# Kernel optimization log

Measured on AMD Instinct MI355X. Metric: run time of the kernel, lower is better.

Reference implementation:

```python
import jax, jax.numpy as jnp
import numpy as np

# dims: N batch, C in-channels, T frames, V joints, H heads, HD per-head dim, O out-channels
N, C, T, V = 32, 64, 256, 25
H, HD, O = 8, 8, 64  # HD = max(C//8, 8)
SCALE = HD ** -0.5
EPS = 1e-5


def setup_inputs() -> dict:
    key = jax.random.key(0)
    ks = jax.random.split(key, 10)
    return {
        "x": jax.random.normal(ks[0], (N, C, T, V), jnp.float32),
        "ln_gamma": jnp.ones((C,), jnp.float32),
        "ln_beta": jnp.zeros((C,), jnp.float32),
        "w_qk": jax.random.normal(ks[1], (C, 2 * H * HD), jnp.float32),  # to_qk init N(0,1)
        "b_qk": jax.random.normal(ks[2], (2 * H * HD,), jnp.float32) * 0.02,
        "shared_topology": jax.random.uniform(ks[3], (H, V, V), jnp.float32),
        "conv_w": jax.random.normal(ks[4], (H, O, C), jnp.float32) * np.sqrt(2.0 / (O * H)),
        "conv_b": jnp.zeros((H, O), jnp.float32),
        "bn_gamma": jnp.full((O,), 1e-6, jnp.float32),
        "bn_beta": jnp.zeros((O,), jnp.float32),
        "bn_mean": jnp.zeros((O,), jnp.float32),
        "bn_var": jnp.ones((O,), jnp.float32),
    }


def reference(x, ln_gamma, ln_beta, w_qk, b_qk, shared_topology,
              conv_w, conv_b, bn_gamma, bn_beta, bn_mean, bn_var):
    # ---- SelfAttention over joints ----
    y = jnp.transpose(x, (0, 2, 3, 1))                 # [N,T,V,C]
    mu = jnp.mean(y, axis=-1, keepdims=True)
    var = jnp.var(y, axis=-1, keepdims=True)
    yn = (y - mu) * jax.lax.rsqrt(var + EPS) * ln_gamma + ln_beta
    qk = yn @ w_qk + b_qk                              # [N,T,V,2*H*HD]
    B = N * T
    q, k = jnp.split(qk.reshape(B, V, 2 * H * HD), 2, axis=-1)
    q = q.reshape(B, V, H, HD).transpose(0, 2, 1, 3)   # [B,H,V,HD]
    k = k.reshape(B, V, H, HD).transpose(0, 2, 1, 3)
    dots = jnp.einsum("bhid,bhjd->bhij", q, k) * SCALE
    attn = jax.nn.softmax(dots, axis=-1).astype(jnp.float32)  # [B,H,V,V]

    # ---- attention-gated graph conv ----
    A = attn * shared_topology[None]                   # [B,H,V,V]
    feat = jnp.transpose(x, (0, 2, 3, 1)).reshape(B, V, C)  # [B,V,C]
    z = jnp.einsum("bhuv,bvc->bhuc", A, feat)          # per-head aggregate [B,H,V,C]
    # fused per-head 1x1 convs + sum over heads
    out = jnp.einsum("bhuc,hoc->buo", z, conv_w) + conv_b.sum(0)  # [B,V,O]
    out = out.reshape(N, T, V, O).transpose(0, 3, 1, 2)           # [N,O,T,V]

    # ---- BatchNorm (inference-mode) + residual + ReLU ----
    g = (bn_gamma * jax.lax.rsqrt(bn_var + EPS))[None, :, None, None]
    b = (bn_beta - bn_mean * bn_gamma * jax.lax.rsqrt(bn_var + EPS))[None, :, None, None]
    out = out * g + b
    out = jax.nn.relu(out + x)  # down is identity (in_c == out_c)
    return out
```

## Files before the change

### kernel.cpp

```cpp
#include <hip/hip_runtime.h>
#include <math.h>

#define SCALE 0.35355339059327373f
#define EPSV 1e-5f

typedef __attribute__((ext_vector_type(8))) short bf16x8;
typedef __attribute__((ext_vector_type(4))) float f32x4;
typedef __attribute__((ext_vector_type(16))) float f32x16;
typedef __attribute__((ext_vector_type(4))) int i32x4;
typedef __attribute__((ext_vector_type(2))) int i32x2;

static __device__ __forceinline__ unsigned short bfh(float f) {
    return (unsigned short)(__builtin_bit_cast(unsigned int, f) >> 16);
}
static __device__ __forceinline__ float bf2f(unsigned short s) {
    return __builtin_bit_cast(float, (unsigned int)s << 16);
}
static __device__ __forceinline__ int pack2(float lo, float hi) {
    return __builtin_amdgcn_perm(__builtin_bit_cast(unsigned int, hi),
                                 __builtin_bit_cast(unsigned int, lo), 0x07060302u);
}
#define LGKM0() __asm__ __volatile__("s_waitcnt lgkmcnt(0)" ::: "memory")

__global__ void prep_kernel(const float* __restrict__ w_qk,
                            const float* __restrict__ conv_w,
                            const float* __restrict__ conv_b,
                            const float* __restrict__ bn_g, const float* __restrict__ bn_b,
                            const float* __restrict__ bn_m, const float* __restrict__ bn_v,
                            unsigned short* __restrict__ ws) {
    int i = blockIdx.x * 256 + threadIdx.x;
    if (i < 8192) {
        int f = i >> 9, rem = i & 511, l = rem >> 3, j = rem & 7;
        int nt = f >> 1, ks = f & 1;
        int k = ks * 32 + (l >> 4) * 8 + j;
        int nn = nt * 16 + (l & 15);
        ws[i] = bfh(w_qk[k * 128 + nn]);
    } else if (i < 40960) {
        int i2 = i - 8192;
        int g = i2 >> 9, rem = i2 & 511, l = rem >> 3, j = rem & 7;
        int h = g >> 3, nt = (g >> 1) & 3, ks = g & 1;
        int c = ks * 32 + (l >> 4) * 8 + j;
        int o = nt * 16 + (l & 15);
        ws[i] = bfh(conv_w[h * 4096 + o * 64 + c]);
    } else if (i < 41024) {
        int o = i - 40960;
        float gv = bn_g[o] * rsqrtf(bn_v[o] + EPSV);
        float bb = bn_b[o] - bn_m[o] * gv;
        float cb = 0.f;
        for (int h = 0; h < 8; h++) cb += conv_b[h * 64 + o];
        float* wsf = (float*)(ws + 40960);
        wsf[o] = gv;
        wsf[64 + o] = bb + cb * gv;
    }
}

__global__ __launch_bounds__(256, 3)
void sagc_kernel(const float* __restrict__ x,
                 const float* __restrict__ ln_g, const float* __restrict__ ln_b,
                 const float* __restrict__ b_qk,
                 const float* __restrict__ topo,
                 const unsigned short* __restrict__ ws,
                 float* __restrict__ out)
{
    __shared__ __align__(16) unsigned char smem[53248];
    const int tid = threadIdx.x;
    const int lane = tid & 63, wv = tid >> 6;
    const int l15 = lane & 15, quad = lane >> 4;
    const int r32 = lane & 31, hi = lane >> 5;

    unsigned char* my = smem + wv * 13312;
    unsigned short* xb16 = (unsigned short*)my;
    unsigned short* FWT  = (unsigned short*)my;
    float*          mus  = (float*)(my + 5120);
    float*          rss  = mus + 32;
    unsigned short* qbuf = (unsigned short*)(my + 5120);
    unsigned short* kbuf = (unsigned short*)(my + 6656);
    unsigned short* Gh   = (unsigned short*)(my + 8192);

    const unsigned short* wqk = ws;
    const unsigned short* w2f = ws + 8192;
    const float* bnA = (const float*)(ws + 40960);
    const float* bnB = bnA + 64;

    const int tile = blockIdx.x * 4 + wv;
    const int n = tile >> 8, t = tile & 255;
    const float* xg = x + (size_t)n * 409600 + (size_t)t * 25;
    float* og = out + (size_t)n * 409600 + (size_t)t * 25;

    #pragma unroll
    for (int it = 0; it < 25; it++) {
        int i = it * 64 + lane;
        int c = i / 25, v = i - c * 25;
        xb16[v * 72 + c] = bfh(xg[c * 6400 + v]);
    }
    #pragma unroll
    for (int k = 0; k < 8; k++) {
        int idx = k * 64 + lane;
        if (idx < 504) {
            int rr = idx / 72, cc = idx - rr * 72;
            xb16[(25 + rr) * 72 + cc] = 0;
        }
    }
    LGKM0();

    bf16x8 xa[2][2];
    #pragma unroll
    for (int mt = 0; mt < 2; mt++)
        #pragma unroll
        for (int ks = 0; ks < 2; ks++)
            xa[mt][ks] = *(const bf16x8*)&xb16[(mt * 16 + l15) * 72 + ks * 32 + quad * 8];

    float xf[2][2][8];
    bf16x8 sqf[2][2];
    #pragma unroll
    for (int mt = 0; mt < 2; mt++)
        #pragma unroll
        for (int ks = 0; ks < 2; ks++) {
            float s[8];
            #pragma unroll
            for (int j = 0; j < 8; j++) {
                xf[mt][ks][j] = bf2f((unsigned short)xa[mt][ks][j]);
                s[j] = xf[mt][ks][j] * xf[mt][ks][j];
            }
            i32x4 p;
            #pragma unroll
            for (int q = 0; q < 4; q++) p[q] = pack2(s[2 * q], s[2 * q + 1]);
            sqf[mt][ks] = __builtin_bit_cast(bf16x8, p);
        }

    {
        i32x4 ones_i = {0x3C803C80, 0x3C803C80, 0x3C803C80, 0x3C803C80};
        bf16x8 onesf = __builtin_bit_cast(bf16x8, ones_i);
        f32x4 z4 = {0.f, 0.f, 0.f, 0.f};
        f32x4 dmu[2], ds2[2];
        #pragma unroll
        for (int mt = 0; mt < 2; mt++) {
            dmu[mt] = __builtin_amdgcn_mfma_f32_16x16x32_bf16(xa[mt][0], onesf, z4, 0, 0, 0);
            dmu[mt] = __builtin_amdgcn_mfma_f32_16x16x32_bf16(xa[mt][1], onesf, dmu[mt], 0, 0, 0);
            ds2[mt] = __builtin_amdgcn_mfma_f32_16x16x32_bf16(sqf[mt][0], onesf, z4, 0, 0, 0);
            ds2[mt] = __builtin_amdgcn_mfma_f32_16x16x32_bf16(sqf[mt][1], onesf, ds2[mt], 0, 0, 0);
        }
        if (l15 == 0) {
            #pragma unroll
            for (int mt = 0; mt < 2; mt++)
                #pragma unroll
                for (int r = 0; r < 4; r++) {
                    int v = mt * 16 + quad * 4 + r;
                    float mu = dmu[mt][r];
                    float var = ds2[mt][r] - mu * mu;
                    mus[v] = mu;
                    rss[v] = rsqrtf(var + EPSV);
                }
        }
    }
    LGKM0();

    bf16x8 yna[2][2];
    {
        float muv[2] = {mus[l15], mus[16 + l15]};
        float rsv[2] = {rss[l15], rss[16 + l15]};
        #pragma unroll
        for (int ks = 0; ks < 2; ks++) {
            f32x4 ga = *(const f32x4*)&ln_g[ks * 32 + quad * 8];
            f32x4 gb = *(const f32x4*)&ln_g[ks * 32 + quad * 8 + 4];
            f32x4 ba = *(const f32x4*)&ln_b[ks * 32 + quad * 8];
            f32x4 bb = *(const f32x4*)&ln_b[ks * 32 + quad * 8 + 4];
            #pragma unroll
            for (int mt = 0; mt < 2; mt++) {
                float yv[8];
                #pragma unroll
                for (int j = 0; j < 8; j++) {
                    float g = (j < 4) ? ga[j] : gb[j - 4];
                    float bt = (j < 4) ? ba[j] : bb[j - 4];
                    yv[j] = (xf[mt][ks][j] - muv[mt]) * rsv[mt] * g + bt;
                }
                i32x4 p;
                #pragma unroll
                for (int q = 0; q < 4; q++) p[q] = pack2(yv[2 * q], yv[2 * q + 1]);
                yna[mt][ks] = __builtin_bit_cast(bf16x8, p);
            }
        }
    }

    f32x4 acc[2][4];
    #pragma unroll
    for (int mt = 0; mt < 2; mt++)
        #pragma unroll
        for (int nt = 0; nt < 4; nt++)
            acc[mt][nt] = (f32x4){0.f, 0.f, 0.f, 0.f};

    const f32x4 z4 = {0.f, 0.f, 0.f, 0.f};
    const bf16x8 z8 = {0, 0, 0, 0, 0, 0, 0, 0};

    for (int hp = 0; hp < 4; hp++) {
        #pragma unroll
        for (int tsel = 0; tsel < 2; tsel++) {
            int nt = tsel ? (4 + hp) : hp;
            bf16x8 b0 = *(const bf16x8*)&wqk[(nt * 2 + 0) * 512 + lane * 8];
            bf16x8 b1 = *(const bf16x8*)&wqk[(nt * 2 + 1) * 512 + lane * 8];
            float bias = b_qk[(tsel ? 64 : 0) + hp * 16 + l15];
            unsigned short* buf = tsel ? kbuf : qbuf;
            #pragma unroll
            for (int mt = 0; mt < 2; mt++) {
                f32x4 d = __builtin_amdgcn_mfma_f32_16x16x32_bf16(yna[mt][0], b0, z4, 0, 0, 0);
                d = __builtin_amdgcn_mfma_f32_16x16x32_bf16(yna[mt][1], b1, d, 0, 0, 0);
                #pragma unroll
                for (int r = 0; r < 4; r++) {
                    int u = mt * 16 + quad * 4 + r;
                    if (u < 25) {
                        float val = d[r] + bias;
                        if (!tsel) val *= SCALE;
                        buf[u * 24 + l15] = bfh(val);
                    }
                }
            }
        }
        LGKM0();

        #pragma unroll
        for (int hh = 0; hh < 2; hh++) {
            bf16x8 aq = z8, bk = z8;
            if (hi == 0) {
                aq = *(const bf16x8*)&qbuf[r32 * 24 + hh * 8];
                bk = *(const bf16x8*)&kbuf[r32 * 24 + hh * 8];
            }
            f32x16 dd = {0.f,0.f,0.f,0.f,0.f,0.f,0.f,0.f,0.f,0.f,0.f,0.f,0.f,0.f,0.f,0.f};
            dd = __builtin_amdgcn_mfma_f32_32x32x16_bf16(aq, bk, dd, 0, 0, 0);
            #pragma unroll
            for (int r = 0; r < 16; r++) {
                int u = (r & 3) + 8 * (r >> 2) + 4 * hi;
                if (u < 25) Gh[hh * 1280 + u * 40 + r32] = bfh(dd[r]);
            }
        }
        LGKM0();

        {
            int smh = lane >> 5, su = lane & 31;
            if (su < 25) {
                unsigned short* rowp = Gh + smh * 1280 + su * 40;
                i32x4 ra = *(const i32x4*)rowp;
                i32x4 rb = *(const i32x4*)(rowp + 8);
                i32x4 rc = *(const i32x4*)(rowp + 16);
                float f[25];
                #pragma unroll
                for (int w = 0; w < 4; w++) {
                    f[2 * w]      = __builtin_bit_cast(float, (unsigned)ra[w] << 16);
                    f[2 * w + 1]  = __builtin_bit_cast(float, (unsigned)ra[w] & 0xFFFF0000u);
                    f[8 + 2 * w]  = __builtin_bit_cast(float, (unsigned)rb[w] << 16);
                    f[9 + 2 * w]  = __builtin_bit_cast(float, (unsigned)rb[w] & 0xFFFF0000u);
                    f[16 + 2 * w] = __builtin_bit_cast(float, (unsigned)rc[w] << 16);
                    f[17 + 2 * w] = __builtin_bit_cast(float, (unsigned)rc[w] & 0xFFFF0000u);
                }
                f[24] = bf2f(rowp[24]);
                float m = f[0];
                #pragma unroll
                for (int v = 1; v < 25; v++) m = fmaxf(m, f[v]);
                float s = 0.f;
                #pragma unroll
                for (int v = 0; v < 25; v++) { f[v] = __expf(f[v] - m); s += f[v]; }
                float inv = 1.0f / s;
                const float* tp = topo + (hp * 2 + smh) * 625 + su * 25;
                #pragma unroll
                for (int v = 0; v < 25; v++) f[v] = f[v] * inv * tp[v];
                int d[16];
                #pragma unroll
                for (int p = 0; p < 12; p++) d[p] = pack2(f[2 * p], f[2 * p + 1]);
                d[12] = pack2(f[24], 0.f);
                d[13] = 0; d[14] = 0; d[15] = 0;
                *(i32x4*)rowp        = (i32x4){d[0], d[1], d[2], d[3]};
                *(i32x4*)(rowp + 8)  = (i32x4){d[4], d[5], d[6], d[7]};
                *(i32x4*)(rowp + 16) = (i32x4){d[8], d[9], d[10], d[11]};
                *(i32x4*)(rowp + 24) = (i32x4){d[12], d[13], d[14], d[15]};
            }
        }
        LGKM0();

        #pragma unroll
        for (int hh = 0; hh < 2; hh++) {
            int h = hp * 2 + hh;
            #pragma unroll
            for (int nt = 0; nt < 4; nt++) {
                bf16x8 w0 = *(const bf16x8*)&w2f[((h * 4 + nt) * 2 + 0) * 512 + lane * 8];
                bf16x8 w1 = *(const bf16x8*)&w2f[((h * 4 + nt) * 2 + 1) * 512 + lane * 8];
                f32x4 dw0 = __builtin_amdgcn_mfma_f32_16x16x32_bf16(xa[0][0], w0, z4, 0, 0, 0);
                dw0 = __builtin_amdgcn_mfma_f32_16x16x32_bf16(xa[0][1], w1, dw0, 0, 0, 0);
                f32x4 dw1 = __builtin_amdgcn_mfma_f32_16x16x32_bf16(xa[1][0], w0, z4, 0, 0, 0);
                dw1 = __builtin_amdgcn_mfma_f32_16x16x32_bf16(xa[1][1], w1, dw1, 0, 0, 0);
                int o = nt * 16 + l15;
                i32x2 q0 = {pack2(dw0[0], dw0[1]), pack2(dw0[2], dw0[3])};
                i32x2 q1 = {pack2(dw1[0], dw1[1]), pack2(dw1[2], dw1[3])};
                *(i32x2*)&FWT[o * 40 + quad * 4] = q0;
                *(i32x2*)&FWT[o * 40 + 16 + quad * 4] = q1;
            }
            LGKM0();
            bf16x8 ag0 = *(const bf16x8*)&Gh[hh * 1280 + l15 * 40 + quad * 8];
            bf16x8 ag1 = *(const bf16x8*)&Gh[hh * 1280 + (16 + l15) * 40 + quad * 8];
            #pragma unroll
            for (int nt = 0; nt < 4; nt++) {
                bf16x8 br = *(const bf16x8*)&FWT[(nt * 16 + l15) * 40 + quad * 8];
                acc[0][nt] = __builtin_amdgcn_mfma_f32_16x16x32_bf16(ag0, br, acc[0][nt], 0, 0, 0);
                acc[1][nt] = __builtin_amdgcn_mfma_f32_16x16x32_bf16(ag1, br, acc[1][nt], 0, 0, 0);
            }
        }
    }

    #pragma unroll
    for (int nt = 0; nt < 4; nt++) {
        int o = nt * 16 + l15;
        float gA = bnA[o], gB = bnB[o];
        #pragma unroll
        for (int mt = 0; mt < 2; mt++) {
            int ub = mt * 16 + quad * 4;
            #pragma unroll
            for (int r = 0; r < 4; r++) {
                int u = ub + r;
                if (u < 25) {
                    float val = acc[mt][nt][r] * gA + gB + xg[o * 6400 + u];
                    og[o * 6400 + u] = fmaxf(val, 0.f);
                }
            }
        }
    }
}

extern "C" void kernel_launch(void* const* d_in, const int* in_sizes, int n_in,
                              void* d_out, int out_size, void* d_ws, size_t ws_size,
                              hipStream_t stream) {
    const float* x      = (const float*)d_in[0];
    const float* ln_g   = (const float*)d_in[1];
    const float* ln_b   = (const float*)d_in[2];
    const float* w_qk   = (const float*)d_in[3];
    const float* b_qk   = (const float*)d_in[4];
    const float* topo   = (const float*)d_in[5];
    const float* conv_w = (const float*)d_in[6];
    const float* conv_b = (const float*)d_in[7];
    const float* bn_g   = (const float*)d_in[8];
    const float* bn_b   = (const float*)d_in[9];
    const float* bn_m   = (const float*)d_in[10];
    const float* bn_v   = (const float*)d_in[11];
    float* outp = (float*)d_out;
    unsigned short* wsp = (unsigned short*)d_ws;

    hipLaunchKernelGGL(prep_kernel, dim3(161), dim3(256), 0, stream,
                       w_qk, conv_w, conv_b, bn_g, bn_b, bn_m, bn_v, wsp);
    hipLaunchKernelGGL(sagc_kernel, dim3(2048), dim3(256), 0, stream,
                       x, ln_g, ln_b, b_qk, topo, (const unsigned short*)wsp, outp);
}
```

Before: 187.5 us.

## Shrink LDS per wave with XOR-swizzled layouts, load x directly to registers

Per-wave shared memory is cut from 13 KB to 8 KB by dropping the LDS staging of x. Each lane now loads its x fragments straight from global memory and packs them to bf16 in registers. The attention and conv-weight buffers switch from padded layouts to 64-byte rows with XOR swizzles to avoid bank conflicts, and launch bounds are raised so more blocks fit per CU. Softmax now uses exp2 with log2e folded into the query scale, tree max reductions, split sums and a hardware reciprocal. The uncoalesced strided global loads of x and the register pressure from the higher occupancy target are the main risks.

```diff
diff --git a/kernel.cpp b/kernel.cpp
--- a/kernel.cpp
+++ b/kernel.cpp
@@ -1,7 +1,7 @@
 #include <hip/hip_runtime.h>
 #include <math.h>
 
-#define SCALE 0.35355339059327373f
+#define SCALE_L2E 0.51006972157f
 #define EPSV 1e-5f
 
 typedef __attribute__((ext_vector_type(8))) short bf16x8;
@@ -54,7 +54,7 @@
     }
 }
 
-__global__ __launch_bounds__(256, 3)
+__global__ __launch_bounds__(256, 5)
 void sagc_kernel(const float* __restrict__ x,
                  const float* __restrict__ ln_g, const float* __restrict__ ln_b,
                  const float* __restrict__ b_qk,
@@ -62,20 +62,19 @@
                  const unsigned short* __restrict__ ws,
                  float* __restrict__ out)
 {
-    __shared__ __align__(16) unsigned char smem[53248];
+    __shared__ __align__(16) unsigned char smem[32768];
     const int tid = threadIdx.x;
     const int lane = tid & 63, wv = tid >> 6;
     const int l15 = lane & 15, quad = lane >> 4;
     const int r32 = lane & 31, hi = lane >> 5;
 
-    unsigned char* my = smem + wv * 13312;
-    unsigned short* xb16 = (unsigned short*)my;
-    unsigned short* FWT  = (unsigned short*)my;
-    float*          mus  = (float*)(my + 5120);
+    unsigned char* my = smem + wv * 8192;
+    unsigned short* qbuf = (unsigned short*)my;
+    unsigned short* kbuf = (unsigned short*)(my + 1536);
+    unsigned char*  fwb  = my;
+    unsigned char*  ghb  = my + 4096;
+    float*          mus  = (float*)(my + 4096);
     float*          rss  = mus + 32;
-    unsigned short* qbuf = (unsigned short*)(my + 5120);
-    unsigned short* kbuf = (unsigned short*)(my + 6656);
-    unsigned short* Gh   = (unsigned short*)(my + 8192);
 
     const unsigned short* wqk = ws;
     const unsigned short* w2f = ws + 8192;
@@ -87,45 +86,35 @@
     const float* xg = x + (size_t)n * 409600 + (size_t)t * 25;
     float* og = out + (size_t)n * 409600 + (size_t)t * 25;
 
+    float xf[2][2][8];
     #pragma unroll
-    for (int it = 0; it < 25; it++) {
-        int i = it * 64 + lane;
-        int c = i / 25, v = i - c * 25;
-        xb16[v * 72 + c] = bfh(xg[c * 6400 + v]);
-    }
-    #pragma unroll
-    for (int k = 0; k < 8; k++) {
-        int idx = k * 64 + lane;
-        if (idx < 504) {
-            int rr = idx / 72, cc = idx - rr * 72;
-            xb16[(25 + rr) * 72 + cc] = 0;
-        }
-    }
-    LGKM0();
-
-    bf16x8 xa[2][2];
+    for (int mt = 0; mt < 2; mt++) {
+        const int v = mt * 16 + l15;
+        const bool ok = (v < 25);
+        const float* xc = xg + v;
+        #pragma unroll
+        for (int ks = 0; ks < 2; ks++)
+            #pragma unroll
+            for (int j = 0; j < 8; j++) {
+                int c = ks * 32 + quad * 8 + j;
+                xf[mt][ks][j] = ok ? xc[c * 6400] : 0.f;
+            }
+    }
+
+    bf16x8 xa[2][2], sqf[2][2];
     #pragma unroll
     for (int mt = 0; mt < 2; mt++)
         #pragma unroll
-        for (int ks = 0; ks < 2; ks++)
-            xa[mt][ks] = *(const bf16x8*)&xb16[(mt * 16 + l15) * 72 + ks * 32 + quad * 8];
-
-    float xf[2][2][8];
-    bf16x8 sqf[2][2];
-    #pragma unroll
-    for (int mt = 0; mt < 2; mt++)
-        #pragma unroll
         for (int ks = 0; ks < 2; ks++) {
-            float s[8];
-            #pragma unroll
-            for (int j = 0; j < 8; j++) {
-                xf[mt][ks][j] = bf2f((unsigned short)xa[mt][ks][j]);
-                s[j] = xf[mt][ks][j] * xf[mt][ks][j];
-            }
-            i32x4 p;
-            #pragma unroll
-            for (int q = 0; q < 4; q++) p[q] = pack2(s[2 * q], s[2 * q + 1]);
-            sqf[mt][ks] = __builtin_bit_cast(bf16x8, p);
+            i32x4 pa, ps;
+            #pragma unroll
+            for (int q = 0; q < 4; q++) {
+                float a = xf[mt][ks][2 * q], b = xf[mt][ks][2 * q + 1];
+                pa[q] = pack2(a, b);
+                ps[q] = pack2(a * a, b * b);
+            }
+            xa[mt][ks]  = __builtin_bit_cast(bf16x8, pa);
+            sqf[mt][ks] = __builtin_bit_cast(bf16x8, ps);
         }
 
     {
@@ -192,6 +181,14 @@
     const f32x4 z4 = {0.f, 0.f, 0.f, 0.f};
     const bf16x8 z8 = {0, 0, 0, 0, 0, 0, 0, 0};
 
+    const int sw4 = (l15 >> 2) & 3;
+    const int blkA = ((r32 >> 3) ^ hi) << 4;
+    unsigned char* gwA = ghb + hi * 256 + (r32 & 7) * 2 + blkA;
+    unsigned char* gwB = ghb + hi * 256 + (r32 & 7) * 2 + (blkA ^ 32);
+    unsigned char* w0p = fwb + ((((quad >> 1) ^ sw4)) << 4) + (quad & 1) * 8;
+    unsigned char* w1p = fwb + (((((quad >> 1) ^ sw4)) ^ 2) << 4) + (quad & 1) * 8;
+    unsigned char* brp = fwb + l15 * 64 + ((quad ^ sw4) << 4);
+
     for (int hp = 0; hp < 4; hp++) {
         #pragma unroll
         for (int tsel = 0; tsel < 2; tsel++) {
@@ -209,7 +206,7 @@
                     int u = mt * 16 + quad * 4 + r;
                     if (u < 25) {
                         float val = d[r] + bias;
-                        if (!tsel) val *= SCALE;
+                        if (!tsel) val *= SCALE_L2E;
                         buf[u * 24 + l15] = bfh(val);
                     }
                 }
@@ -228,8 +225,11 @@
             dd = __builtin_amdgcn_mfma_f32_32x32x16_bf16(aq, bk, dd, 0, 0, 0);
             #pragma unroll
             for (int r = 0; r < 16; r++) {
-                int u = (r & 3) + 8 * (r >> 2) + 4 * hi;
-                if (u < 25) Gh[hh * 1280 + u * 40 + r32] = bfh(dd[r]);
+                int ub = (r & 3) + 8 * (r >> 2);
+                if (ub + 4 * hi < 25) {
+                    unsigned char* p = (((r >> 2) & 1) ? gwB : gwA) + hh * 2048 + ub * 64;
+                    *(unsigned short*)p = bfh(dd[r]);
+                }
             }
         }
         LGKM0();
@@ -237,10 +237,11 @@
         {
             int smh = lane >> 5, su = lane & 31;
             if (su < 25) {
-                unsigned short* rowp = Gh + smh * 1280 + su * 40;
-                i32x4 ra = *(const i32x4*)rowp;
-                i32x4 rb = *(const i32x4*)(rowp + 8);
-                i32x4 rc = *(const i32x4*)(rowp + 16);
+                unsigned char* rowb = ghb + smh * 2048 + su * 64;
+                int sz = ((su >> 2) & 3) << 4;
+                i32x4 ra = *(const i32x4*)(rowb + (sz ^ 0));
+                i32x4 rb = *(const i32x4*)(rowb + (sz ^ 16));
+                i32x4 rc = *(const i32x4*)(rowb + (sz ^ 32));
                 float f[25];
                 #pragma unroll
                 for (int w = 0; w < 4; w++) {
@@ -251,26 +252,34 @@
                     f[16 + 2 * w] = __builtin_bit_cast(float, (unsigned)rc[w] << 16);
                     f[17 + 2 * w] = __builtin_bit_cast(float, (unsigned)rc[w] & 0xFFFF0000u);
                 }
-                f[24] = bf2f(rowp[24]);
-                float m = f[0];
-                #pragma unroll
-                for (int v = 1; v < 25; v++) m = fmaxf(m, f[v]);
-                float s = 0.f;
-                #pragma unroll
-                for (int v = 0; v < 25; v++) { f[v] = __expf(f[v] - m); s += f[v]; }
-                float inv = 1.0f / s;
+                f[24] = bf2f(*(const unsigned short*)(rowb + (sz ^ 48)));
+                float g12[12];
+                #pragma unroll
+                for (int i2 = 0; i2 < 12; i2++) g12[i2] = fmaxf(f[i2], f[i2 + 12]);
+                #pragma unroll
+                for (int i2 = 0; i2 < 6; i2++) g12[i2] = fmaxf(g12[i2], g12[i2 + 6]);
+                float m = fmaxf(fmaxf(fmaxf(g12[0], g12[1]), fmaxf(g12[2], g12[3])),
+                                fmaxf(fmaxf(g12[4], g12[5]), f[24]));
+                float s0 = 0.f, s1 = 0.f, s2 = 0.f, s3 = 0.f;
+                #pragma unroll
+                for (int v = 0; v < 24; v += 4) {
+                    f[v]     = __builtin_amdgcn_exp2f(f[v] - m);     s0 += f[v];
+                    f[v + 1] = __builtin_amdgcn_exp2f(f[v + 1] - m); s1 += f[v + 1];
+                    f[v + 2] = __builtin_amdgcn_exp2f(f[v + 2] - m); s2 += f[v + 2];
+                    f[v + 3] = __builtin_amdgcn_exp2f(f[v + 3] - m); s3 += f[v + 3];
+                }
+                f[24] = __builtin_amdgcn_exp2f(f[24] - m);
+                float inv = __builtin_amdgcn_rcpf(((s0 + s1) + (s2 + s3)) + f[24]);
                 const float* tp = topo + (hp * 2 + smh) * 625 + su * 25;
                 #pragma unroll
                 for (int v = 0; v < 25; v++) f[v] = f[v] * inv * tp[v];
-                int d[16];
+                int d[12];
                 #pragma unroll
                 for (int p = 0; p < 12; p++) d[p] = pack2(f[2 * p], f[2 * p + 1]);
-                d[12] = pack2(f[24], 0.f);
-                d[13] = 0; d[14] = 0; d[15] = 0;
-                *(i32x4*)rowp        = (i32x4){d[0], d[1], d[2], d[3]};
-                *(i32x4*)(rowp + 8)  = (i32x4){d[4], d[5], d[6], d[7]};
-                *(i32x4*)(rowp + 16) = (i32x4){d[8], d[9], d[10], d[11]};
-                *(i32x4*)(rowp + 24) = (i32x4){d[12], d[13], d[14], d[15]};
+                *(i32x4*)(rowb + (sz ^ 0))  = (i32x4){d[0], d[1], d[2], d[3]};
+                *(i32x4*)(rowb + (sz ^ 16)) = (i32x4){d[4], d[5], d[6], d[7]};
+                *(i32x4*)(rowb + (sz ^ 32)) = (i32x4){d[8], d[9], d[10], d[11]};
+                *(i32x4*)(rowb + (sz ^ 48)) = (i32x4){pack2(f[24], 0.f), 0, 0, 0};
             }
         }
         LGKM0();
@@ -286,18 +295,18 @@
                 dw0 = __builtin_amdgcn_mfma_f32_16x16x32_bf16(xa[0][1], w1, dw0, 0, 0, 0);
                 f32x4 dw1 = __builtin_amdgcn_mfma_f32_16x16x32_bf16(xa[1][0], w0, z4, 0, 0, 0);
                 dw1 = __builtin_amdgcn_mfma_f32_16x16x32_bf16(xa[1][1], w1, dw1, 0, 0, 0);
-                int o = nt * 16 + l15;
                 i32x2 q0 = {pack2(dw0[0], dw0[1]), pack2(dw0[2], dw0[3])};
                 i32x2 q1 = {pack2(dw1[0], dw1[1]), pack2(dw1[2], dw1[3])};
-                *(i32x2*)&FWT[o * 40 + quad * 4] = q0;
-                *(i32x2*)&FWT[o * 40 + 16 + quad * 4] = q1;
+                *(i32x2*)(w0p + nt * 1024 + l15 * 64) = q0;
+                *(i32x2*)(w1p + nt * 1024 + l15 * 64) = q1;
             }
             LGKM0();
-            bf16x8 ag0 = *(const bf16x8*)&Gh[hh * 1280 + l15 * 40 + quad * 8];
-            bf16x8 ag1 = *(const bf16x8*)&Gh[hh * 1280 + (16 + l15) * 40 + quad * 8];
+            unsigned char* agp = ghb + hh * 2048 + l15 * 64 + ((quad ^ sw4) << 4);
+            bf16x8 ag0 = *(const bf16x8*)agp;
+            bf16x8 ag1 = *(const bf16x8*)(agp + 1024);
             #pragma unroll
             for (int nt = 0; nt < 4; nt++) {
-                bf16x8 br = *(const bf16x8*)&FWT[(nt * 16 + l15) * 40 + quad * 8];
+                bf16x8 br = *(const bf16x8*)(brp + nt * 1024);
                 acc[0][nt] = __builtin_amdgcn_mfma_f32_16x16x32_bf16(ag0, br, acc[0][nt], 0, 0, 0);
                 acc[1][nt] = __builtin_amdgcn_mfma_f32_16x16x32_bf16(ag1, br, acc[1][nt], 0, 0, 0);
             }
```

After: 263.9 us. 40.7% more time.
